# Optimization experiments

Hardware: AMD Instinct MI355X
Metric: run time of the kernel (lower is better)

Reference implementation:

```python
import jax, jax.numpy as jnp
import numpy as np

N = 50000   # nodes of ntype 'A'
E = 800000  # edges per metapath
M = 4       # metapaths (first-order, tail = 'A')
H = 4       # attn heads
C = 32      # out_channels = output_dim // attn_heads
IN = 256    # input_dim
D = H * C   # output_dim = 128
NEG_SLOPE = 0.2


def setup_inputs() -> dict:
    key = jax.random.key(0)
    ks = jax.random.split(key, 8)
    feats = jax.random.normal(ks[0], (N, IN), dtype=jnp.float32)
    edge_index = jax.random.randint(ks[1], (M, 2, E), 0, N, dtype=jnp.int32)
    W = jax.random.normal(ks[2], (IN, D), dtype=jnp.float32) * (2.0 / (IN + D)) ** 0.5
    b = jnp.zeros((D,), dtype=jnp.float32)
    attn = jax.random.normal(ks[3], (M, H, 2 * C), dtype=jnp.float32) * 0.1
    rel_attn_l = jax.random.normal(ks[4], (H, C), dtype=jnp.float32) * 0.1
    rel_attn_r = jax.random.normal(ks[5], (M + 1, H, C), dtype=jnp.float32) * 0.1
    rel_attn_bias = jnp.zeros((M + 1,), dtype=jnp.float32)
    return {"feats": feats, "edge_index": edge_index, "W": W, "b": b,
            "attn": attn, "rel_attn_l": rel_attn_l, "rel_attn_r": rel_attn_r,
            "rel_attn_bias": rel_attn_bias}


def _segment_softmax(logits, seg, num_segments):
    # logits: [E, H], seg: [E] target-node ids; softmax over incoming edges per node.
    seg_max = jax.ops.segment_max(logits, seg, num_segments=num_segments)  # [N, H]
    e = jnp.exp(logits - seg_max[seg])
    seg_sum = jax.ops.segment_sum(e, seg, num_segments=num_segments)       # [N, H]
    return e / (seg_sum[seg] + 1e-16)


def reference(feats, edge_index, W, b, attn, rel_attn_l, rel_attn_r, rel_attn_bias):
    # projection: per-ntype Linear + relu, reshape to heads
    h = jax.nn.relu(feats @ W + b).reshape(N, H, C)  # l_dict == r_dict == h

    # per-metapath GAT-style propagate (aggr='add')
    rels = []
    for m in range(M):
        src = edge_index[m, 0]
        dst = edge_index[m, 1]
        x_j = h[src]  # [E, H, C] source messages
        x_i = h[dst]  # [E, H, C] target queries
        # alpha = (cat([x_i, x_j], -1) * attn[m]).sum(-1), LeakyReLU(0.2)
        logits = jnp.einsum('ehc,hc->eh', x_i, attn[m, :, :C]) \
               + jnp.einsum('ehc,hc->eh', x_j, attn[m, :, C:])
        logits = jax.nn.leaky_relu(logits, NEG_SLOPE)
        alpha = _segment_softmax(logits, dst, N)                 # [E, H]
        out = jax.ops.segment_sum(x_j * alpha[..., None], dst, num_segments=N)  # [N, H, C]
        rels.append(out)
    rels.append(h)  # last relation slot = self (embedding[:, -1] = l_dict[ntype])
    emb = jnp.stack(rels, axis=1)  # [N, M+1, H, C]

    # beta relation-attention weights
    beta_l = jax.nn.relu(h * rel_attn_l)                          # [N, H, C]
    beta_r = jax.nn.relu(emb * rel_attn_r)                        # [N, M+1, H, C]
    beta = jnp.einsum('nhc,nrhc->nrh', beta_l, beta_r) + rel_attn_bias[None, :, None]
    beta = jax.nn.softmax(beta, axis=1)                           # over relations

    emb = (emb * beta[..., None]).sum(axis=1).reshape(N, D)
    return jax.nn.relu(emb)
```

## Files before the change

kernel.cpp:

```cpp
#include <hip/hip_runtime.h>
#include <math.h>

#define kN 50000
#define kE 800000
#define kM 4
#define kH 4
#define kC 32
#define kIN 256
#define kD 128

typedef __attribute__((ext_vector_type(8))) short bf16x8;
typedef __attribute__((ext_vector_type(4))) float f32x4;

__device__ __forceinline__ unsigned int f2bf_pack(float a, float b) {
    unsigned ua = __float_as_uint(a);
    ua += 0x7fffu + ((ua >> 16) & 1u);
    unsigned ub = __float_as_uint(b);
    ub += 0x7fffu + ((ub >> 16) & 1u);
    return (ua >> 16) | (ub & 0xffff0000u);
}
__device__ __forceinline__ unsigned short f2bf(float x) {
    unsigned u = __float_as_uint(x);
    u += 0x7fffu + ((u >> 16) & 1u);
    return (unsigned short)(u >> 16);
}

#define NBK 98
#define BCAP 10240
#define MW (NBK * BCAP)
#define PAB ((kE + 4095) / 4096)

__global__ void k_wcast(const float* __restrict__ W, unsigned short* __restrict__ Wt16) {
    const int col = blockIdx.x;
    const int k = threadIdx.x;
    Wt16[(size_t)col * kIN + k] = f2bf(W[(size_t)k * kD + col]);
}

#define GEMMB ((kN + 127) / 128)
__global__ __launch_bounds__(256) void k_gemmbucket(const float* __restrict__ feats,
                                                    const unsigned short* __restrict__ Wt16,
                                                    const float* __restrict__ b,
                                                    const float* __restrict__ attn,
                                                    unsigned short* __restrict__ h16,
                                                    float* __restrict__ sl,
                                                    float* __restrict__ sr,
                                                    const int* __restrict__ ei,
                                                    int* __restrict__ bcur,
                                                    unsigned int* __restrict__ pairs) {
    __shared__ unsigned short fr16[128 * 32];
    __shared__ unsigned short hlds[128][130];
    __shared__ int hist[NBK], h2[NBK], base_s[NBK];
    const int t = threadIdx.x;

    if (blockIdx.x >= GEMMB) {
        const int bi = blockIdx.x - GEMMB;
        const int m = bi / PAB;
        const int chunk = bi - m * PAB;
        const int e0 = chunk * 4096;
        for (int j = t; j < NBK; j += 256) { hist[j] = 0; h2[j] = 0; }
        __syncthreads();
        int src[16], dst[16];
#pragma unroll
        for (int i = 0; i < 16; i++) {
            const int e = e0 + i * 256 + t;
            const int eok = (e < kE) ? e : 0;
            src[i] = ei[(size_t)m * 2 * kE + eok];
            dst[i] = (e < kE) ? ei[(size_t)m * 2 * kE + kE + eok] : -1;
        }
#pragma unroll
        for (int i = 0; i < 16; i++)
            if (dst[i] >= 0) atomicAdd(&hist[dst[i] >> 9], 1);
        __syncthreads();
        for (int j = t; j < NBK; j += 256)
            base_s[j] = atomicAdd(&bcur[m * NBK + j], hist[j]);
        __syncthreads();
#pragma unroll
        for (int i = 0; i < 16; i++) {
            if (dst[i] >= 0) {
                const int bk = dst[i] >> 9;
                const int slot = base_s[bk] + atomicAdd(&h2[bk], 1);
                pairs[(size_t)m * MW + (size_t)bk * BCAP + slot] =
                    ((unsigned int)(dst[i] & 511) << 16) | (unsigned int)src[i];
            }
        }
        return;
    }

    const int lane = t & 63;
    const int wave = t >> 6;
    const int q = lane >> 4;
    const int m16 = lane & 15;
    const int wrow = (wave >> 1) * 64;
    const int wcol = (wave & 1) * 64;
    const int rowbase = blockIdx.x * 128;

    f32x4 acc[4][4];
#pragma unroll
    for (int i = 0; i < 4; i++)
#pragma unroll
        for (int j = 0; j < 4; j++) acc[i][j] = (f32x4){0.f, 0.f, 0.f, 0.f};

    const int srow = t >> 3;
    const int sk4 = t & 7;

    for (int kc = 0; kc < kIN; kc += 32) {
        __syncthreads();
#pragma unroll
        for (int it = 0; it < 4; it++) {
            const int row = srow + it * 32;
            const int rg = rowbase + row;
            float4 v = make_float4(0.f, 0.f, 0.f, 0.f);
            if (rg < kN)
                v = *reinterpret_cast<const float4*>(feats + (size_t)rg * kIN + kc + sk4 * 4);
            uint2 p;
            p.x = f2bf_pack(v.x, v.y);
            p.y = f2bf_pack(v.z, v.w);
            *reinterpret_cast<uint2*>(&fr16[row * 32 + sk4 * 4]) = p;
        }
        __syncthreads();

        bf16x8 afr[4], bfr[4];
#pragma unroll
        for (int ri = 0; ri < 4; ri++)
            afr[ri] = *reinterpret_cast<const bf16x8*>(
                &fr16[(wrow + ri * 16 + m16) * 32 + q * 8]);
#pragma unroll
        for (int ci = 0; ci < 4; ci++)
            bfr[ci] = *reinterpret_cast<const bf16x8*>(
                Wt16 + (size_t)(wcol + ci * 16 + m16) * kIN + kc + q * 8);
#pragma unroll
        for (int ri = 0; ri < 4; ri++)
#pragma unroll
            for (int ci = 0; ci < 4; ci++)
                acc[ri][ci] = __builtin_amdgcn_mfma_f32_16x16x32_bf16(
                    afr[ri], bfr[ci], acc[ri][ci], 0, 0, 0);
    }

    float bcol[4];
#pragma unroll
    for (int ci = 0; ci < 4; ci++) bcol[ci] = b[wcol + ci * 16 + m16];

#pragma unroll
    for (int ri = 0; ri < 4; ri++) {
#pragma unroll
        for (int reg = 0; reg < 4; reg++) {
            const int row = wrow + ri * 16 + q * 4 + reg;
            const int rg = rowbase + row;
#pragma unroll
            for (int ci = 0; ci < 4; ci++) {
                const int col = wcol + ci * 16 + m16;
                const float v = fmaxf(acc[ri][ci][reg] + bcol[ci], 0.f);
                const unsigned short us = f2bf(v);
                hlds[row][col] = us;
                if (rg < kN)
                    h16[(size_t)rg * kD + col] = us;
            }
        }
    }
    __syncthreads();

    const unsigned int* hl32 = reinterpret_cast<const unsigned int*>(&hlds[0][0]);
#pragma unroll
    for (int it = 0; it < 2; it++) {
        const int task = it * 256 + t;
        const int hh = task & 3;
        const int nl = task >> 2;
        const int n = rowbase + nl;
        if (n < kN) {
            unsigned int u[16];
#pragma unroll
            for (int k = 0; k < 16; k++) u[k] = hl32[nl * 65 + hh * 16 + k];
            float f0[16], f1[16];
#pragma unroll
            for (int k = 0; k < 16; k++) {
                f0[k] = __uint_as_float(u[k] << 16);
                f1[k] = __uint_as_float(u[k] & 0xffff0000u);
            }
#pragma unroll
            for (int m = 0; m < kM; m++) {
                const float2* al = reinterpret_cast<const float2*>(attn + (m * kH + hh) * 2 * kC);
                const float2* ar = al + 16;
                float s0 = 0.f, s1 = 0.f;
#pragma unroll
                for (int k = 0; k < 16; k++) {
                    const float2 a = al[k], r = ar[k];
                    s0 += f0[k] * a.x + f1[k] * a.y;
                    s1 += f0[k] * r.x + f1[k] * r.y;
                }
                sl[((size_t)m * kN + n) * kH + hh] = s0;
                sr[((size_t)m * kN + n) * kH + hh] = s1;
            }
        }
    }
}

#define SORTB (kM * NBK)
__global__ __launch_bounds__(256) void k_sort(const unsigned int* __restrict__ pairs,
                                              const int* __restrict__ bcur,
                                              int* __restrict__ offs,
                                              int* __restrict__ cnta,
                                              int* __restrict__ srcsort) {
    __shared__ int hist[512], pref[512], h2[512], wt[4];
    const int t = threadIdx.x;
    const int m = blockIdx.x / NBK;
    const int bk = blockIdx.x - m * NBK;
    const int bs = bk << 9;
    const int base = bk * BCAP;
    const int n = bcur[m * NBK + bk];
    const unsigned int* __restrict__ pb = pairs + (size_t)m * MW + base;
    int* __restrict__ ss = srcsort + (size_t)m * MW + base;

    hist[t] = 0; hist[t + 256] = 0; h2[t] = 0; h2[t + 256] = 0;
    __syncthreads();

    unsigned int v[40];
#pragma unroll
    for (int j = 0; j < 40; j++) {
        const int idx = j * 256 + t;
        v[j] = (idx < n) ? pb[idx] : 0xffffffffu;
    }
#pragma unroll
    for (int j = 0; j < 40; j++)
        if (v[j] != 0xffffffffu) atomicAdd(&hist[v[j] >> 16], 1);
    __syncthreads();

    const int lane = t & 63, wid = t >> 6;
    const int j0 = 2 * t, j1 = 2 * t + 1;
    const int h0 = hist[j0], h1 = hist[j1];
    const int s = h0 + h1;
    int incl = s;
#pragma unroll
    for (int d = 1; d < 64; d <<= 1) {
        const int x = __shfl_up(incl, d);
        if (lane >= d) incl += x;
    }
    if (lane == 63) wt[wid] = incl;
    __syncthreads();
    int woff = 0;
#pragma unroll
    for (int i = 0; i < 4; i++)
        if (i < wid) woff += wt[i];
    const int excl = woff + incl - s;
    pref[j0] = excl;
    pref[j1] = excl + h0;
    const int d0 = bs + j0, d1 = bs + j1;
    if (d0 < kN) { offs[m * kN + d0] = base + excl;       cnta[m * kN + d0] = h0; }
    if (d1 < kN) { offs[m * kN + d1] = base + excl + h0;  cnta[m * kN + d1] = h1; }
    __syncthreads();

#pragma unroll
    for (int j = 0; j < 40; j++) {
        if (v[j] != 0xffffffffu) {
            const int dl = (int)(v[j] >> 16);
            const int pos = pref[dl] + atomicAdd(&h2[dl], 1);
            ss[pos] = (int)(v[j] & 0xffffu);
        }
    }
}

#define CH 16

#define AGG_BODY(GN)                                                            \
    {                                                                           \
        int sj[GN];                                                             \
        _Pragma("unroll")                                                       \
        for (int j = 0; j < GN; j++) {                                          \
            const int id = __builtin_amdgcn_readlane(my0, j);                   \
            sj[j] = (j < nb) ? id : dst;                                        \
        }                                                                       \
        unsigned int u[GN];                                                     \
        _Pragma("unroll")                                                       \
        for (int j = 0; j < GN; j++)                                            \
            u[j] = *reinterpret_cast<const unsigned int*>(                      \
                hb + (((size_t)(unsigned int)sj[j] << 8) + ebyte));             \
        float x = sl_h + srv;                                                   \
        x = x > 0.f ? x : 0.2f * x;                         \
        const float w = (c + jj < cnt) ? __expf(x) : 0.f;                       \
        sum += w;                                                               \
        swts[m][l] = w;                                                         \
        __builtin_amdgcn_wave_barrier();                                        \
        const float4 w0 = *reinterpret_cast<const float4*>(&swts[m][hh * 16]);  \
        const float4 w1 = *reinterpret_cast<const float4*>(&swts[m][hh*16+4]);  \
        const float4 w2 = *reinterpret_cast<const float4*>(&swts[m][hh*16+8]);  \
        const float4 w3 = *reinterpret_cast<const float4*>(&swts[m][hh*16+12]); \
        __builtin_amdgcn_wave_barrier();                                        \
        my0 = my1;                                                              \
        my1 = sbase[c + 2 * CH + jj];                                           \
        srv = *reinterpret_cast<const float*>(                                  \
            srb + (((unsigned int)my0 << 4) + hbyte));                          \
        const float wj[16] = {w0.x, w0.y, w0.z, w0.w, w1.x, w1.y, w1.z, w1.w,   \
                              w2.x, w2.y, w2.z, w2.w, w3.x, w3.y, w3.z, w3.w};  \
        _Pragma("unroll")                                                       \
        for (int j = 0; j < GN; j++) {                                          \
            a0 += wj[j] * __uint_as_float(u[j] << 16);                          \
            a1 += wj[j] * __uint_as_float(u[j] & 0xffff0000u);                  \
        }                                                                       \
    }

__global__ __launch_bounds__(256) void k_agg(const unsigned short* __restrict__ h16,
                                             const float* __restrict__ sl,
                                             const float* __restrict__ sr,
                                             const int* __restrict__ offs,
                                             const int* __restrict__ cnta,
                                             const int* __restrict__ srcsort,
                                             const float* __restrict__ ral,
                                             const float* __restrict__ rar,
                                             const float* __restrict__ rbias,
                                             float* __restrict__ out) {
    const int dst = blockIdx.x;
    const int t = threadIdx.x;
    const int m = t >> 6;
    const int l = t & 63;
    const int hh = l >> 4;
    const int jj = l & 15;
    const int e0 = l * 2;

    __shared__ float smres[kM][kD];
    __shared__ float swts[kM][64];

    const int beg = offs[m * kN + dst];
    const int cnt = cnta[m * kN + dst];
    const float sl_h = sl[((size_t)m * kN + dst) * kH + hh];
    const int* __restrict__ sbase = srcsort + (size_t)m * MW + beg;
    const char* __restrict__ hb = (const char*)h16;
    const char* __restrict__ srb = (const char*)(sr + (size_t)m * kN * kH);
    const unsigned int ebyte = (unsigned int)(e0 << 1);
    const unsigned int hbyte = (unsigned int)(hh << 2);

    float sum = 0.f, a0 = 0.f, a1 = 0.f;

    int my0 = sbase[jj];
    int my1 = sbase[CH + jj];
    float srv = *reinterpret_cast<const float*>(
        srb + (((unsigned int)my0 << 4) + hbyte));

    for (int c = 0; c < cnt; c += CH) {
        const int nb = cnt - c;
        if (nb >= 9) AGG_BODY(16) else AGG_BODY(8)
    }

    sum += __shfl_xor(sum, 1);
    sum += __shfl_xor(sum, 2);
    sum += __shfl_xor(sum, 4);
    sum += __shfl_xor(sum, 8);
    const float inv = 1.0f / (sum + 1e-16f);
    smres[m][e0] = a0 * inv;
    smres[m][e0 + 1] = a1 * inv;
    __syncthreads();

    if (m == 0) {
        const unsigned int ud = *reinterpret_cast<const unsigned int*>(
            hb + (((unsigned int)dst << 8) + ebyte));
        const float hd0 = __uint_as_float(ud << 16);
        const float hd1 = __uint_as_float(ud & 0xffff0000u);
        const float bl0 = fmaxf(hd0 * ral[e0], 0.f);
        const float bl1 = fmaxf(hd1 * ral[e0 + 1], 0.f);
        float emb0[5], emb1[5], beta[5];
#pragma unroll
        for (int r = 0; r < 5; r++) {
            const float x0 = (r < 4) ? smres[r][e0] : hd0;
            const float x1 = (r < 4) ? smres[r][e0 + 1] : hd1;
            emb0[r] = x0;
            emb1[r] = x1;
            const float br0 = fmaxf(x0 * rar[r * kD + e0], 0.f);
            const float br1 = fmaxf(x1 * rar[r * kD + e0 + 1], 0.f);
            float p = bl0 * br0 + bl1 * br1;
            p += __shfl_xor(p, 1);
            p += __shfl_xor(p, 2);
            p += __shfl_xor(p, 4);
            p += __shfl_xor(p, 8);
            beta[r] = p + rbias[r];
        }
        float mx = beta[0];
#pragma unroll
        for (int r = 1; r < 5; r++) mx = fmaxf(mx, beta[r]);
        float s = 0.f, wgt[5];
#pragma unroll
        for (int r = 0; r < 5; r++) { wgt[r] = __expf(beta[r] - mx); s += wgt[r]; }
        const float invb = 1.f / s;
        float o0 = 0.f, o1 = 0.f;
#pragma unroll
        for (int r = 0; r < 5; r++) { o0 += emb0[r] * wgt[r]; o1 += emb1[r] * wgt[r]; }
        out[(size_t)dst * kD + e0] = fmaxf(o0 * invb, 0.f);
        out[(size_t)dst * kD + e0 + 1] = fmaxf(o1 * invb, 0.f);
    }
}

extern "C" void kernel_launch(void* const* d_in, const int* in_sizes, int n_in,
                              void* d_out, int out_size, void* d_ws, size_t ws_size,
                              hipStream_t stream) {
    const float* feats = (const float*)d_in[0];
    const int* ei      = (const int*)d_in[1];
    const float* W     = (const float*)d_in[2];
    const float* b     = (const float*)d_in[3];
    const float* attn  = (const float*)d_in[4];
    const float* ral   = (const float*)d_in[5];
    const float* rar   = (const float*)d_in[6];
    const float* rbias = (const float*)d_in[7];
    float* out = (float*)d_out;

    char* ws = (char*)d_ws;
    size_t off = 0;
    auto alloc = [&](size_t bytes) -> void* {
        void* p = ws + off;
        off = (off + bytes + 255) & ~(size_t)255;
        return p;
    };
    unsigned short* h16 = (unsigned short*)alloc(sizeof(short) * (size_t)kN * kD);
    unsigned short* Wt16= (unsigned short*)alloc(sizeof(short) * (size_t)kD * kIN);
    float* sl   = (float*)alloc(sizeof(float) * (size_t)kM * kN * kH);
    float* sr   = (float*)alloc(sizeof(float) * (size_t)kM * kN * kH);
    int* cnta   = (int*)alloc(sizeof(int) * (size_t)kM * kN);
    int* offs   = (int*)alloc(sizeof(int) * (size_t)kM * kN);
    int* bcur   = (int*)alloc(sizeof(int) * (kM * NBK + 64));
    int* srcsort= (int*)alloc(sizeof(int) * ((size_t)kM * MW + 64));
    unsigned int* pairs = (unsigned int*)alloc(sizeof(int) * (size_t)kM * MW);

    hipMemsetAsync(bcur, 0, sizeof(int) * (kM * NBK + 64), stream);
    hipMemsetAsync(srcsort, 0, sizeof(int) * ((size_t)kM * MW + 64), stream);
    k_wcast<<<kD, kIN, 0, stream>>>(W, Wt16);
    k_gemmbucket<<<GEMMB + kM * PAB, 256, 0, stream>>>(feats, Wt16, b, attn,
                                                       h16, sl, sr, ei, bcur, pairs);
    k_sort<<<SORTB, 256, 0, stream>>>(pairs, bcur, offs, cnta, srcsort);
    k_agg<<<kN, 256, 0, stream>>>(h16, sl, sr, offs, cnta, srcsort,
                                  ral, rar, rbias, out);
}
```

Measured before the change: 349.5 us.

## Shrink sorted source indices to 16-bit, halve GEMM LDS, drop srcsort memset

Sorted per-bucket source indices are now stored as 16-bit values instead of 32-bit, which halves index traffic in the sort and aggregation kernels. The full-buffer memset of srcsort is removed, and the sort kernel instead zeroes the 64 slots past each bucket's end so the aggregation prefetch reads valid indices. The GEMM kernel reuses a single smaller LDS buffer and processes the bf16 tile in two 64-row halves with extra barriers, aiming for lower LDS use and higher occupancy. Storing the source in 16 bits silently drops the high bit because N is 50000 and can exceed 65535? No: 50000 fits in 16 bits, so this relies on N staying below 65536.

```diff
diff --git a/kernel.cpp b/kernel.cpp
--- a/kernel.cpp
+++ b/kernel.cpp
@@ -47,8 +47,7 @@
                                                     const int* __restrict__ ei,
                                                     int* __restrict__ bcur,
                                                     unsigned int* __restrict__ pairs) {
-    __shared__ unsigned short fr16[128 * 32];
-    __shared__ unsigned short hlds[128][130];
+    __shared__ __align__(16) unsigned char smem[64 * 130 * 2];
     __shared__ int hist[NBK], h2[NBK], base_s[NBK];
     const int t = threadIdx.x;
 
@@ -85,6 +84,10 @@
         }
         return;
     }
+
+    unsigned short* fr16 = reinterpret_cast<unsigned short*>(smem);
+    typedef unsigned short hrow_t[130];
+    hrow_t* hlds = reinterpret_cast<hrow_t*>(smem);
 
     const int lane = t & 63;
     const int wave = t >> 6;
@@ -146,51 +149,67 @@
         for (int reg = 0; reg < 4; reg++) {
             const int row = wrow + ri * 16 + q * 4 + reg;
             const int rg = rowbase + row;
-#pragma unroll
-            for (int ci = 0; ci < 4; ci++) {
-                const int col = wcol + ci * 16 + m16;
-                const float v = fmaxf(acc[ri][ci][reg] + bcol[ci], 0.f);
-                const unsigned short us = f2bf(v);
-                hlds[row][col] = us;
-                if (rg < kN)
-                    h16[(size_t)rg * kD + col] = us;
+            if (rg < kN) {
+#pragma unroll
+                for (int ci = 0; ci < 4; ci++) {
+                    const int col = wcol + ci * 16 + m16;
+                    const float v = fmaxf(acc[ri][ci][reg] + bcol[ci], 0.f);
+                    h16[(size_t)rg * kD + col] = f2bf(v);
+                }
             }
         }
     }
     __syncthreads();
 
-    const unsigned int* hl32 = reinterpret_cast<const unsigned int*>(&hlds[0][0]);
-#pragma unroll
-    for (int it = 0; it < 2; it++) {
-        const int task = it * 256 + t;
-        const int hh = task & 3;
-        const int nl = task >> 2;
-        const int n = rowbase + nl;
-        if (n < kN) {
-            unsigned int u[16];
-#pragma unroll
-            for (int k = 0; k < 16; k++) u[k] = hl32[nl * 65 + hh * 16 + k];
-            float f0[16], f1[16];
-#pragma unroll
-            for (int k = 0; k < 16; k++) {
-                f0[k] = __uint_as_float(u[k] << 16);
-                f1[k] = __uint_as_float(u[k] & 0xffff0000u);
+    const unsigned int* hl32 = reinterpret_cast<const unsigned int*>(smem);
+#pragma unroll
+    for (int half = 0; half < 2; half++) {
+        if ((wrow >> 6) == half) {
+#pragma unroll
+            for (int ri = 0; ri < 4; ri++)
+#pragma unroll
+                for (int reg = 0; reg < 4; reg++) {
+                    const int row = (wrow & 63) + ri * 16 + q * 4 + reg;
+#pragma unroll
+                    for (int ci = 0; ci < 4; ci++) {
+                        const int col = wcol + ci * 16 + m16;
+                        const float v = fmaxf(acc[ri][ci][reg] + bcol[ci], 0.f);
+                        hlds[row][col] = f2bf(v);
+                    }
+                }
+        }
+        __syncthreads();
+        {
+            const int hh = t & 3;
+            const int nl = t >> 2;
+            const int n = rowbase + half * 64 + nl;
+            if (n < kN) {
+                unsigned int u[16];
+#pragma unroll
+                for (int k = 0; k < 16; k++) u[k] = hl32[nl * 65 + hh * 16 + k];
+                float f0[16], f1[16];
+#pragma unroll
+                for (int k = 0; k < 16; k++) {
+                    f0[k] = __uint_as_float(u[k] << 16);
+                    f1[k] = __uint_as_float(u[k] & 0xffff0000u);
+                }
+#pragma unroll
+                for (int m = 0; m < kM; m++) {
+                    const float2* al = reinterpret_cast<const float2*>(attn + (m * kH + hh) * 2 * kC);
+                    const float2* ar = al + 16;
+                    float s0 = 0.f, s1 = 0.f;
+#pragma unroll
+                    for (int k = 0; k < 16; k++) {
+                        const float2 a = al[k], r = ar[k];
+                        s0 += f0[k] * a.x + f1[k] * a.y;
+                        s1 += f0[k] * r.x + f1[k] * r.y;
+                    }
+                    sl[((size_t)m * kN + n) * kH + hh] = s0;
+                    sr[((size_t)m * kN + n) * kH + hh] = s1;
+                }
             }
-#pragma unroll
-            for (int m = 0; m < kM; m++) {
-                const float2* al = reinterpret_cast<const float2*>(attn + (m * kH + hh) * 2 * kC);
-                const float2* ar = al + 16;
-                float s0 = 0.f, s1 = 0.f;
-#pragma unroll
-                for (int k = 0; k < 16; k++) {
-                    const float2 a = al[k], r = ar[k];
-                    s0 += f0[k] * a.x + f1[k] * a.y;
-                    s1 += f0[k] * r.x + f1[k] * r.y;
-                }
-                sl[((size_t)m * kN + n) * kH + hh] = s0;
-                sr[((size_t)m * kN + n) * kH + hh] = s1;
-            }
-        }
+        }
+        __syncthreads();
     }
 }
 
@@ -199,7 +218,7 @@
                                               const int* __restrict__ bcur,
                                               int* __restrict__ offs,
                                               int* __restrict__ cnta,
-                                              int* __restrict__ srcsort) {
+                                              unsigned short* __restrict__ srcsort) {
     __shared__ int hist[512], pref[512], h2[512], wt[4];
     const int t = threadIdx.x;
     const int m = blockIdx.x / NBK;
@@ -208,7 +227,7 @@
     const int base = bk * BCAP;
     const int n = bcur[m * NBK + bk];
     const unsigned int* __restrict__ pb = pairs + (size_t)m * MW + base;
-    int* __restrict__ ss = srcsort + (size_t)m * MW + base;
+    unsigned short* __restrict__ ss = srcsort + (size_t)m * MW + base;
 
     hist[t] = 0; hist[t + 256] = 0; h2[t] = 0; h2[t + 256] = 0;
     __syncthreads();
@@ -253,9 +272,10 @@
         if (v[j] != 0xffffffffu) {
             const int dl = (int)(v[j] >> 16);
             const int pos = pref[dl] + atomicAdd(&h2[dl], 1);
-            ss[pos] = (int)(v[j] & 0xffffu);
-        }
-    }
+            ss[pos] = (unsigned short)(v[j] & 0xffffu);
+        }
+    }
+    if (t < 64 && n + t < BCAP) ss[n + t] = 0;
 }
 
 #define CH 16
@@ -302,7 +322,7 @@
                                              const float* __restrict__ sr,
                                              const int* __restrict__ offs,
                                              const int* __restrict__ cnta,
-                                             const int* __restrict__ srcsort,
+                                             const unsigned short* __restrict__ srcsort,
                                              const float* __restrict__ ral,
                                              const float* __restrict__ rar,
                                              const float* __restrict__ rbias,
@@ -321,7 +341,7 @@
     const int beg = offs[m * kN + dst];
     const int cnt = cnta[m * kN + dst];
     const float sl_h = sl[((size_t)m * kN + dst) * kH + hh];
-    const int* __restrict__ sbase = srcsort + (size_t)m * MW + beg;
+    const unsigned short* __restrict__ sbase = srcsort + (size_t)m * MW + beg;
     const char* __restrict__ hb = (const char*)h16;
     const char* __restrict__ srb = (const char*)(sr + (size_t)m * kN * kH);
     const unsigned int ebyte = (unsigned int)(e0 << 1);
@@ -413,11 +433,11 @@
     int* cnta   = (int*)alloc(sizeof(int) * (size_t)kM * kN);
     int* offs   = (int*)alloc(sizeof(int) * (size_t)kM * kN);
     int* bcur   = (int*)alloc(sizeof(int) * (kM * NBK + 64));
-    int* srcsort= (int*)alloc(sizeof(int) * ((size_t)kM * MW + 64));
+    unsigned short* srcsort =
+        (unsigned short*)alloc(sizeof(short) * ((size_t)kM * MW + 64));
     unsigned int* pairs = (unsigned int*)alloc(sizeof(int) * (size_t)kM * MW);
 
     hipMemsetAsync(bcur, 0, sizeof(int) * (kM * NBK + 64), stream);
-    hipMemsetAsync(srcsort, 0, sizeof(int) * ((size_t)kM * MW + 64), stream);
     k_wcast<<<kD, kIN, 0, stream>>>(W, Wt16);
     k_gemmbucket<<<GEMMB + kM * PAB, 256, 0, stream>>>(feats, Wt16, b, attn,
                                                        h16, sl, sr, ei, bcur, pairs);
```

After: 341.4 us (median of 2 runs). 2.3% less time.
